# Performance work log

Measured on AMD Instinct MI355X. Metric: run time of the kernel, lower is better.

Reference implementation:

```python
import jax, jax.numpy as jnp
import numpy as np

B = 256          # graphs per batch
NC, NP = 16384, 131072   # compound / protein node counts
EC, EP = 131072, 2097152 # edge counts
D = 128


def _gconv(x, src, dst, W, b, n):
    # DGL GraphConv, norm='both': h = D_in^{-1/2} A D_out^{-1/2} x W + b
    ones = jnp.ones(src.shape, x.dtype)
    out_deg = jax.ops.segment_sum(ones, src, num_segments=n)
    in_deg = jax.ops.segment_sum(ones, dst, num_segments=n)
    ns = jax.lax.rsqrt(jnp.maximum(out_deg, 1.0))
    nd = jax.lax.rsqrt(jnp.maximum(in_deg, 1.0))
    h = (x * ns[:, None]) @ W           # apply weight before aggregation (same math, less traffic)
    m = jax.ops.segment_sum(h[src], dst, num_segments=n)  # SpMM aggregation
    return m * nd[:, None] + b


def _mean_nodes(x, gid, nb):
    s = jax.ops.segment_sum(x, gid, num_segments=nb)
    cnt = jax.ops.segment_sum(jnp.ones((x.shape[0],), x.dtype), gid, num_segments=nb)
    return s / jnp.maximum(cnt, 1.0)[:, None]


def setup_inputs() -> dict:
    key = jax.random.key(0)
    ks = jax.random.split(key, 24)
    s = 0.05
    inp = {
        "compound_feat": jax.random.normal(ks[0], (NC, 74), jnp.float32),
        "protein_feat": jax.random.normal(ks[1], (NP, 128), jnp.float32),
        # graph structure
        "c_src": jax.random.randint(ks[2], (EC,), 0, NC, jnp.int32),
        "c_dst": jax.random.randint(ks[3], (EC,), 0, NC, jnp.int32),
        "p_src": jax.random.randint(ks[4], (EP,), 0, NP, jnp.int32),
        "p_dst": jax.random.randint(ks[5], (EP,), 0, NP, jnp.int32),
        "c_gid": jax.random.randint(ks[6], (NC,), 0, B, jnp.int32),
        "p_gid": jax.random.randint(ks[7], (NP,), 0, B, jnp.int32),
        # GraphConv params
        "Wc1": jax.random.normal(ks[8], (74, D), jnp.float32) * s,
        "bc1": jnp.zeros((D,), jnp.float32),
        "Wc2": jax.random.normal(ks[9], (D, D), jnp.float32) * s,
        "bc2": jnp.zeros((D,), jnp.float32),
        "Wp1": jax.random.normal(ks[10], (128, D), jnp.float32) * s,
        "bp1": jnp.zeros((D,), jnp.float32),
        "Wp2": jax.random.normal(ks[11], (D, D), jnp.float32) * s,
        "bp2": jnp.zeros((D,), jnp.float32),
        # predictor MLP
        "Wf1": jax.random.normal(ks[12], (2 * D, D), jnp.float32) * s,
        "bf1": jnp.zeros((D,), jnp.float32),
        "Wf2": jax.random.normal(ks[13], (D, 1), jnp.float32) * s,
        "bf2": jnp.zeros((1,), jnp.float32),
    }
    return inp


def reference(compound_feat, protein_feat, c_src, c_dst, p_src, p_dst, c_gid, p_gid,
              Wc1, bc1, Wc2, bc2, Wp1, bp1, Wp2, bp2, Wf1, bf1, Wf2, bf2):
    c = jax.nn.relu(_gconv(compound_feat, c_src, c_dst, Wc1, bc1, NC))
    c = jax.nn.relu(_gconv(c, c_src, c_dst, Wc2, bc2, NC))
    c_global = _mean_nodes(c, c_gid, B)                     # [B, D]
    p = jax.nn.relu(_gconv(protein_feat, p_src, p_dst, Wp1, bp1, NP))
    p = jax.nn.relu(_gconv(p, p_src, p_dst, Wp2, bp2, NP))
    p_global = _mean_nodes(p, p_gid, B)                     # [B, D]
    combined = jnp.concatenate([c_global, p_global], axis=1)  # [B, 2D]
    h = jax.nn.relu(combined @ Wf1 + bf1)
    out = h @ Wf2 + bf2                                     # [B, 1]
    return out.squeeze(-1)
```

## Files before the change

kernel.cpp:

```cpp
#include <hip/hip_runtime.h>
#include <hip/hip_fp16.h>

#define D 128
#define SCH 4096
#define NBLK 256

typedef _Float16 half8 __attribute__((ext_vector_type(8)));
typedef float f32x4 __attribute__((ext_vector_type(4)));

struct HTask { const int* keys; int n; int shift; int* H; };
struct H6 { HTask t[6]; };

struct SPTask { const int* in; int n; int* part; };
struct SP6 { SPTask t[6]; };

struct SDTask { const int* in; int n; const int* part; int* out; int* total; };
struct SD6 { SDTask t[6]; };

struct ScTask { const int* k1; const int* k2; int n; int shift;
                const int* base1; const int* base2;
                int* o1; int* o2k; int* o2v; int mode; };
struct Sc4 { ScTask t[4]; };

struct CTask { const int* tmpk; const int* base; int n; int fine; int* deg; };
struct C4 { CTask t[4]; };

struct NTask { const int* outdeg; const int* indeg; float* ns; float* nd; int n; };
struct N2 { NTask t[2]; };

struct LTask { const int* tmpk; const int* tmpv; const int* base; int n;
               const int* rowptr; int shift; int fine; int* col; };
struct L2T { LTask t[2]; };

struct WPk { const float* W; _Float16* out; int K; };
struct W4 { WPk t[4]; };

struct GTask { const void* x; const float* ns; const _Float16* Wp; __half* h;
               int K; int xh; };
struct GemP { GTask t[2]; int nb0; };

struct ATask { const __half* h; const int* rowptr; const int* col;
               const float* nd; const float* b; const int* perm;
               void* out; int halfOut; };
struct AggP { ATask t[2]; int np; int ntot; };

struct MTask { const __half* x; const int* gbase; int n; float* out; };
struct M2 { MTask t[2]; };


__global__ __launch_bounds__(256) void k_hist_all(H6 P) {
  HTask tk = P.t[blockIdx.y];
  __shared__ int bins[256];
  int blk = blockIdx.x, t = threadIdx.x;
  bins[t] = 0;
  __syncthreads();
  int per = (tk.n + NBLK - 1) / NBLK;
  int beg = blk * per, end = min(beg + per, tk.n);
  for (int i = beg + t; i < end; i += 256)
    atomicAdd(&bins[tk.keys[i] >> tk.shift], 1);
  __syncthreads();
  tk.H[t * NBLK + blk] = bins[t];
}

__global__ __launch_bounds__(256) void k_scan_part_all(SP6 P) {
  SPTask tk = P.t[blockIdx.y];
  int b = blockIdx.x, t = threadIdx.x;
  int base = b * SCH;
  int s = 0;
  for (int i = t; i < SCH; i += 256) {
    int idx = base + i;
    if (idx < tk.n) s += tk.in[idx];
  }
  __shared__ int red[256];
  red[t] = s;
  __syncthreads();
  for (int d = 128; d > 0; d >>= 1) {
    if (t < d) red[t] += red[t + d];
    __syncthreads();
  }
  if (t == 0) tk.part[b] = red[0];
}

__global__ __launch_bounds__(256) void k_scan_down_all(SD6 P) {
  SDTask tk = P.t[blockIdx.y];
  int b = blockIdx.x, t = threadIdx.x;
  int lane = t & 63, wid = t >> 6;
  __shared__ int wsum[4];
  if (b == 0 && t == 0 && tk.total) {
    int s = 0;
    for (int w = 0; w < (int)gridDim.x; ++w) s += tk.part[w];
    *tk.total = s;
  }
  int offset = 0;
  for (int w = 0; w < b; ++w) offset += tk.part[w];
  int base = b * SCH;
  if (base >= tk.n) return;
  int idx0 = base + t * 16;
  int v[16];
  int s = 0;
#pragma unroll
  for (int i = 0; i < 16; ++i) {
    int idx = idx0 + i;
    v[i] = (idx < tk.n) ? tk.in[idx] : 0;
    s += v[i];
  }
  int inc = s;
  for (int d = 1; d < 64; d <<= 1) {
    int u = __shfl_up(inc, d, 64);
    if (lane >= d) inc += u;
  }
  if (lane == 63) wsum[wid] = inc;
  __syncthreads();
  int woff = 0;
  for (int w = 0; w < wid; ++w) woff += wsum[w];
  int ex = offset + woff + inc - s;
#pragma unroll
  for (int i = 0; i < 16; ++i) {
    int idx = idx0 + i;
    if (idx < tk.n) tk.out[idx] = ex;
    ex += v[i];
  }
}

__global__ __launch_bounds__(256) void k_scatter_all(Sc4 P) {
  ScTask tk = P.t[blockIdx.y];
  __shared__ int curA[256], curB[256];
  int blk = blockIdx.x, t = threadIdx.x;
  curA[t] = tk.base1[t * NBLK + blk];
  if (tk.mode == 0) curB[t] = tk.base2[t * NBLK + blk];
  __syncthreads();
  int per = (tk.n + NBLK - 1) / NBLK;
  int beg = blk * per, end = min(beg + per, tk.n);
  if (tk.mode == 0) {
    for (int i = beg + t; i < end; i += 256) {
      int s = tk.k1[i], d = tk.k2[i];
      int pa = atomicAdd(&curA[s >> tk.shift], 1);
      tk.o1[pa] = s;
      int pb = atomicAdd(&curB[d >> tk.shift], 1);
      tk.o2k[pb] = d;
      tk.o2v[pb] = s;
    }
  } else {
    for (int i = beg + t; i < end; i += 256) {
      int pa = atomicAdd(&curA[tk.k1[i] >> tk.shift], 1);
      tk.o1[i] = pa;
    }
  }
}

__global__ __launch_bounds__(256) void k_l2count_all(C4 P) {
  CTask tk = P.t[blockIdx.y];
  __shared__ int bins[512];
  int b = blockIdx.x, t = threadIdx.x;
  for (int f = t; f < tk.fine; f += 256) bins[f] = 0;
  __syncthreads();
  int beg = tk.base[b * NBLK];
  int end = (b == NBLK - 1) ? tk.n : tk.base[(b + 1) * NBLK];
  for (int i = beg + t; i < end; i += 256)
    atomicAdd(&bins[tk.tmpk[i] & (tk.fine - 1)], 1);
  __syncthreads();
  for (int f = t; f < tk.fine; f += 256)
    tk.deg[b * tk.fine + f] = bins[f];
}

__global__ __launch_bounds__(256) void k_norms_all(N2 P) {
  NTask tk = P.t[blockIdx.y];
  int i = blockIdx.x * blockDim.x + threadIdx.x;
  if (i < tk.n) {
    tk.ns[i] = rsqrtf(fmaxf((float)tk.outdeg[i], 1.f));
    tk.nd[i] = rsqrtf(fmaxf((float)tk.indeg[i], 1.f));
  }
}

__global__ __launch_bounds__(256) void k_l2scatter_all(L2T P) {
  LTask tk = P.t[blockIdx.y];
  __shared__ int cur[512];
  int b = blockIdx.x, t = threadIdx.x;
  int v0 = b << tk.shift;
  for (int f = t; f < tk.fine; f += 256) cur[f] = tk.rowptr[v0 + f];
  __syncthreads();
  int beg = tk.base[b * NBLK];
  int end = (b == NBLK - 1) ? tk.n : tk.base[(b + 1) * NBLK];
  for (int i = beg + t; i < end; i += 256) {
    int pos = atomicAdd(&cur[tk.tmpk[i] & (tk.fine - 1)], 1);
    tk.col[pos] = tk.tmpv[i];
  }
}


__global__ __launch_bounds__(256) void k_wpack(W4 P) {
  WPk tk = P.t[blockIdx.y];
  int f = blockIdx.x;
  int kch = (tk.K + 31) >> 5;
  if (f >= (kch << 3)) return;
  int kc = f >> 3, nt = f & 7;
  int t = threadIdx.x;
  int l = t & 63, e0 = (t >> 6) << 1;
  int col = (nt << 4) + (l & 15);
  int kb = (kc << 5) + ((l >> 4) << 3);
#pragma unroll
  for (int e = e0; e < e0 + 2; ++e) {
    int k = kb + e;
    float v = (k < tk.K) ? tk.W[(size_t)k * D + col] : 0.f;
    tk.out[(((size_t)f * 64 + l) << 3) + e] = (_Float16)v;
  }
}

__global__ __launch_bounds__(256) void k_nl_gemm(GemP P) {
  __shared__ __align__(16) _Float16 Bs[32 * 64 * 8];
  int bx = blockIdx.x;
  GTask tk;
  int v0;
  if (bx < P.nb0) { tk = P.t[0]; v0 = bx * 128; }
  else            { tk = P.t[1]; v0 = (bx - P.nb0) * 128; }
  const int K = tk.K;
  const int kch = (K + 31) >> 5;
  int t = threadIdx.x, w = t >> 6, l = t & 63;

  {
    const uint4* src = (const uint4*)tk.Wp;
    uint4* dst = (uint4*)Bs;
    int n16 = kch << 9;
    for (int i = t; i < n16; i += 256) dst[i] = src[i];
  }
  __syncthreads();

  int row = l & 15;
  int ks = (l >> 4) << 3;
  int m0 = v0 + (w << 5);
  const float* xf0 = nullptr; const float* xf1 = nullptr;
  const _Float16* xh0 = nullptr; const _Float16* xh1 = nullptr;
  if (tk.xh) {
    xh0 = (const _Float16*)tk.x + (size_t)(m0 + row) * D + ks;
    xh1 = xh0 + (size_t)16 * D;
  } else {
    xf0 = (const float*)tk.x + (size_t)(m0 + row) * K + ks;
    xf1 = xf0 + (size_t)16 * K;
  }

  f32x4 acc[2][8];
  f32x4 zero = {0.f, 0.f, 0.f, 0.f};
#pragma unroll
  for (int i = 0; i < 2; ++i)
#pragma unroll
    for (int j = 0; j < 8; ++j) acc[i][j] = zero;

  for (int kc = 0; kc < kch; ++kc) {
    half8 a0, a1;
    if (tk.xh) {
      a0 = *(const half8*)(xh0 + (kc << 5));
      a1 = *(const half8*)(xh1 + (kc << 5));
    } else if (K == D) {
      float4 p0 = *(const float4*)(xf0 + (kc << 5));
      float4 p1 = *(const float4*)(xf0 + (kc << 5) + 4);
      float4 q0 = *(const float4*)(xf1 + (kc << 5));
      float4 q1 = *(const float4*)(xf1 + (kc << 5) + 4);
      a0[0] = (_Float16)p0.x; a0[1] = (_Float16)p0.y;
      a0[2] = (_Float16)p0.z; a0[3] = (_Float16)p0.w;
      a0[4] = (_Float16)p1.x; a0[5] = (_Float16)p1.y;
      a0[6] = (_Float16)p1.z; a0[7] = (_Float16)p1.w;
      a1[0] = (_Float16)q0.x; a1[1] = (_Float16)q0.y;
      a1[2] = (_Float16)q0.z; a1[3] = (_Float16)q0.w;
      a1[4] = (_Float16)q1.x; a1[5] = (_Float16)q1.y;
      a1[6] = (_Float16)q1.z; a1[7] = (_Float16)q1.w;
    } else {
#pragma unroll
      for (int e = 0; e < 8; ++e) {
        int k = (kc << 5) + ks + e;
        a0[e] = (k < K) ? (_Float16)xf0[(kc << 5) + e] : (_Float16)0.f;
        a1[e] = (k < K) ? (_Float16)xf1[(kc << 5) + e] : (_Float16)0.f;
      }
    }
#pragma unroll
    for (int nt = 0; nt < 8; ++nt) {
      half8 b = *(const half8*)&Bs[(size_t)((((kc << 3) + nt) << 6) + l) << 3];
      acc[0][nt] = __builtin_amdgcn_mfma_f32_16x16x32_f16(a0, b, acc[0][nt], 0, 0, 0);
      acc[1][nt] = __builtin_amdgcn_mfma_f32_16x16x32_f16(a1, b, acc[1][nt], 0, 0, 0);
    }
  }

  int rr = (l >> 4) << 2;
  int c0 = l & 15;
#pragma unroll
  for (int mt = 0; mt < 2; ++mt) {
    int vb = m0 + (mt << 4) + rr;
    float s0 = tk.ns[vb], s1 = tk.ns[vb + 1];
    float s2 = tk.ns[vb + 2], s3 = tk.ns[vb + 3];
#pragma unroll
    for (int nt = 0; nt < 8; ++nt) {
      __half* hp = tk.h + (size_t)vb * D + (nt << 4) + c0;
      hp[0]     = __float2half_rn(acc[mt][nt][0] * s0);
      hp[D]     = __float2half_rn(acc[mt][nt][1] * s1);
      hp[2 * D] = __float2half_rn(acc[mt][nt][2] * s2);
      hp[3 * D] = __float2half_rn(acc[mt][nt][3] * s3);
    }
  }
}

__global__ __launch_bounds__(256) void k_aggregate(AggP P) {
  int wid = threadIdx.x >> 6;
  int lane = threadIdx.x & 63;
  int f0 = (lane & 15) * 8;
  int rsel = lane >> 4;
  int nw = (int)gridDim.x * 4;

  for (int gv = blockIdx.x * 4 + wid; gv < P.ntot; gv += nw) {
    ATask tk;
    int v;
    if (gv < P.np) { tk = P.t[0]; v = gv; }
    else           { tk = P.t[1]; v = gv - P.np; }
    int beg = tk.rowptr[v], end = tk.rowptr[v + 1];
    const __half* h = tk.h;
    const int* col = tk.col;

    float acc[8];
#pragma unroll
    for (int k = 0; k < 8; ++k) acc[k] = 0.f;

    for (int j = beg; j < end; j += 32) {
      int cc[8];
#pragma unroll
      for (int q = 0; q < 8; ++q) {
        int jj = j + 4 * q + rsel;
        cc[q] = (jj < end) ? col[jj] : -1;
      }
#pragma unroll
      for (int q = 0; q < 8; ++q) {
        if (cc[q] >= 0) {
          uint4 r = *(const uint4*)&h[(size_t)cc[q] * D + f0];
          const __half2* p = (const __half2*)&r;
#pragma unroll
          for (int k = 0; k < 4; ++k) {
            float2 f = __half22float2(p[k]);
            acc[2 * k] += f.x; acc[2 * k + 1] += f.y;
          }
        }
      }
    }

#pragma unroll
    for (int k = 0; k < 8; ++k) {
      acc[k] += __shfl_down(acc[k], 32, 64);
      acc[k] += __shfl_down(acc[k], 16, 64);
    }

    if (rsel == 0) {
      float s = tk.nd[v];
      float4 b0 = *(const float4*)&tk.b[f0];
      float4 b1 = *(const float4*)&tk.b[f0 + 4];
      float r[8];
      r[0] = fmaxf(fmaf(acc[0], s, b0.x), 0.f);
      r[1] = fmaxf(fmaf(acc[1], s, b0.y), 0.f);
      r[2] = fmaxf(fmaf(acc[2], s, b0.z), 0.f);
      r[3] = fmaxf(fmaf(acc[3], s, b0.w), 0.f);
      r[4] = fmaxf(fmaf(acc[4], s, b1.x), 0.f);
      r[5] = fmaxf(fmaf(acc[5], s, b1.y), 0.f);
      r[6] = fmaxf(fmaf(acc[6], s, b1.z), 0.f);
      r[7] = fmaxf(fmaf(acc[7], s, b1.w), 0.f);
      int ov = tk.perm ? tk.perm[v] : v;
      if (tk.halfOut) {
        union { __half2 h2[4]; uint4 u; } pk;
#pragma unroll
        for (int k = 0; k < 4; ++k) {
          pk.h2[k].x = __float2half_rn(r[2 * k]);
          pk.h2[k].y = __float2half_rn(r[2 * k + 1]);
        }
        *(uint4*)&((__half*)tk.out)[(size_t)ov * D + f0] = pk.u;
      } else {
        float4 o0 = {r[0], r[1], r[2], r[3]};
        float4 o1 = {r[4], r[5], r[6], r[7]};
        *(float4*)&((float*)tk.out)[(size_t)ov * D + f0] = o0;
        *(float4*)&((float*)tk.out)[(size_t)ov * D + f0 + 4] = o1;
      }
    }
  }
}

__device__ __forceinline__ void acc_half4(float4& a, const __half* p) {
  uint2 r = *(const uint2*)p;
  __half2 q0 = *(__half2*)&r.x;
  __half2 q1 = *(__half2*)&r.y;
  float2 f0 = __half22float2(q0);
  float2 f1 = __half22float2(q1);
  a.x += f0.x; a.y += f0.y; a.z += f1.x; a.w += f1.y;
}

__global__ __launch_bounds__(256) void k_seg_mean(M2 P) {
  MTask tk = P.t[blockIdx.y];
  int g = blockIdx.x, t = threadIdx.x;
  int slot = t >> 5;
  int c = (t & 31) * 4;
  int beg = tk.gbase[g * NBLK];
  int end = (g == (int)gridDim.x - 1) ? tk.n : tk.gbase[(g + 1) * NBLK];
  const __half* x = tk.x;

  float4 a0 = make_float4(0.f, 0.f, 0.f, 0.f);
  float4 a1 = make_float4(0.f, 0.f, 0.f, 0.f);
  int j = beg + slot;
  for (; j + 8 < end; j += 16) {
    acc_half4(a0, x + (size_t)j * D + c);
    acc_half4(a1, x + (size_t)(j + 8) * D + c);
  }
  if (j < end)
    acc_half4(a0, x + (size_t)j * D + c);
  a0.x += a1.x; a0.y += a1.y; a0.z += a1.z; a0.w += a1.w;

  a0.x += __shfl_down(a0.x, 32, 64);
  a0.y += __shfl_down(a0.y, 32, 64);
  a0.z += __shfl_down(a0.z, 32, 64);
  a0.w += __shfl_down(a0.w, 32, 64);

  __shared__ float sred[4][32 * 4];
  int wid = t >> 6, lane = t & 63;
  if (lane < 32) *(float4*)&sred[wid][lane * 4] = a0;
  __syncthreads();
  if (t < 32) {
    float4 s0 = *(const float4*)&sred[0][t * 4];
    float4 s1 = *(const float4*)&sred[1][t * 4];
    float4 s2 = *(const float4*)&sred[2][t * 4];
    float4 s3 = *(const float4*)&sred[3][t * 4];
    float inv = 1.f / fmaxf((float)(end - beg), 1.f);
    float4 r;
    r.x = (s0.x + s1.x + s2.x + s3.x) * inv;
    r.y = (s0.y + s1.y + s2.y + s3.y) * inv;
    r.z = (s0.z + s1.z + s2.z + s3.z) * inv;
    r.w = (s0.w + s1.w + s2.w + s3.w) * inv;
    *(float4*)&tk.out[(size_t)g * D + c] = r;
  }
}

__global__ void k_mlp(const float* __restrict__ cg, const float* __restrict__ pg,
                      const float* __restrict__ Wf1, const float* __restrict__ bf1,
                      const float* __restrict__ Wf2, const float* __restrict__ bf2,
                      float* __restrict__ out) {
  __shared__ float xs[256];
  __shared__ float red[128];
  int b = blockIdx.x, t = threadIdx.x;
  xs[t] = cg[b * D + t];
  xs[128 + t] = pg[b * D + t];
  __syncthreads();
  float acc = bf1[t];
  for (int k = 0; k < 256; ++k) acc = fmaf(xs[k], Wf1[k * D + t], acc);
  float hv = fmaxf(acc, 0.f);
  red[t] = hv * Wf2[t];
  for (int d = 64; d > 0; d >>= 1) {
    __syncthreads();
    if (t < d) red[t] += red[t + d];
  }
  if (t == 0) out[b] = red[0] + bf2[0];
}


extern "C" void kernel_launch(void* const* d_in, const int* in_sizes, int n_in,
                              void* d_out, int out_size, void* d_ws, size_t ws_size,
                              hipStream_t stream) {
  const float* compound_feat = (const float*)d_in[0];
  const float* protein_feat  = (const float*)d_in[1];
  const int* c_src = (const int*)d_in[2];
  const int* c_dst = (const int*)d_in[3];
  const int* p_src = (const int*)d_in[4];
  const int* p_dst = (const int*)d_in[5];
  const int* c_gid = (const int*)d_in[6];
  const int* p_gid = (const int*)d_in[7];
  const float* Wc1 = (const float*)d_in[8];  const float* bc1 = (const float*)d_in[9];
  const float* Wc2 = (const float*)d_in[10]; const float* bc2 = (const float*)d_in[11];
  const float* Wp1 = (const float*)d_in[12]; const float* bp1 = (const float*)d_in[13];
  const float* Wp2 = (const float*)d_in[14]; const float* bp2 = (const float*)d_in[15];
  const float* Wf1 = (const float*)d_in[16]; const float* bf1 = (const float*)d_in[17];
  const float* Wf2 = (const float*)d_in[18]; const float* bf2 = (const float*)d_in[19];
  float* out = (float*)d_out;

  const int EC = in_sizes[2], EP = in_sizes[4];
  const int NC = in_sizes[6], NP = in_sizes[7];
  const int B  = out_size;
  const int KC = in_sizes[0] / NC;
  const int cshift = __builtin_ctz(NC / 256), cfine = NC / 256;
  const int pshift = __builtin_ctz(NP / 256), pfine = NP / 256;
  const int HN = 256 * NBLK;

  char* ws = (char*)d_ws;
  size_t off = 0;
  auto alloc = [&](size_t bytes) -> void* {
    void* p = ws + off;
    off += (bytes + 255) & ~(size_t)255;
    return p;
  };

  int* H0 = (int*)alloc((size_t)HN * 4);
  int* H1 = (int*)alloc((size_t)HN * 4);
  int* H2 = (int*)alloc((size_t)HN * 4);
  int* H3 = (int*)alloc((size_t)HN * 4);
  int* H4 = (int*)alloc((size_t)HN * 4);
  int* H5 = (int*)alloc((size_t)HN * 4);
  int* partH = (int*)alloc((size_t)6 * 32 * 4);
  int* partD = (int*)alloc((size_t)2 * 32 * 4);
  int* tmps_c = (int*)alloc((size_t)EC * 4);
  int* tmpd_c = (int*)alloc((size_t)EC * 4);
  int* tmpv_c = (int*)alloc((size_t)EC * 4);
  int* tmps_p = (int*)alloc((size_t)EP * 4);
  int* tmpd_p = (int*)alloc((size_t)EP * 4);
  int* tmpv_p = (int*)alloc((size_t)EP * 4);
  int* c_outdeg = (int*)alloc((size_t)NC * 4);
  int* c_indeg  = (int*)alloc((size_t)NC * 4);
  int* p_outdeg = (int*)alloc((size_t)NP * 4);
  int* p_indeg  = (int*)alloc((size_t)NP * 4);
  float* c_ns = (float*)alloc((size_t)NC * 4);
  float* c_nd = (float*)alloc((size_t)NC * 4);
  float* p_ns = (float*)alloc((size_t)NP * 4);
  float* p_nd = (float*)alloc((size_t)NP * 4);
  int* c_rowptr = (int*)alloc((size_t)(NC + 1) * 4);
  int* p_rowptr = (int*)alloc((size_t)(NP + 1) * 4);
  int* c_col   = (int*)alloc((size_t)EC * 4);
  int* p_col   = (int*)alloc((size_t)EP * 4);
  int* c_perm = (int*)alloc((size_t)NC * 4);
  int* p_perm = (int*)alloc((size_t)NP * 4);
  __half* c_h  = (__half*)alloc((size_t)NC * D * 2);
  __half* c_m1 = (__half*)alloc((size_t)NC * D * 2);
  __half* c_m2 = (__half*)alloc((size_t)NC * D * 2);
  __half* p_h  = (__half*)alloc((size_t)NP * D * 2);
  __half* p_m1 = (__half*)alloc((size_t)NP * D * 2);
  __half* p_m2 = (__half*)alloc((size_t)NP * D * 2);
  float* cg = (float*)alloc((size_t)B * D * 4);
  float* pg = (float*)alloc((size_t)B * D * 4);
  _Float16* wp_p1 = (_Float16*)alloc((size_t)32 * 1024);
  _Float16* wp_c1 = (_Float16*)alloc((size_t)32 * 1024);
  _Float16* wp_p2 = (_Float16*)alloc((size_t)32 * 1024);
  _Float16* wp_c2 = (_Float16*)alloc((size_t)32 * 1024);
  (void)ws_size; (void)n_in;

  {
    W4 PW = {{{Wp1, wp_p1, D}, {Wc1, wp_c1, KC}, {Wp2, wp_p2, D}, {Wc2, wp_c2, D}}};
    k_wpack<<<dim3(32, 4), 256, 0, stream>>>(PW);
  }
  {
    H6 P = {{{c_src, EC, cshift, H0}, {c_dst, EC, cshift, H1}, {c_gid, NC, 0, H2},
             {p_src, EP, pshift, H3}, {p_dst, EP, pshift, H4}, {p_gid, NP, 0, H5}}};
    k_hist_all<<<dim3(NBLK, 6), 256, 0, stream>>>(P);
  }
  {
    SP6 Pp = {{{H0, HN, partH + 0}, {H1, HN, partH + 32}, {H2, HN, partH + 64},
               {H3, HN, partH + 96}, {H4, HN, partH + 128}, {H5, HN, partH + 160}}};
    k_scan_part_all<<<dim3(16, 6), 256, 0, stream>>>(Pp);
    SD6 Pd = {{{H0, HN, partH + 0, H0, nullptr}, {H1, HN, partH + 32, H1, nullptr},
               {H2, HN, partH + 64, H2, nullptr}, {H3, HN, partH + 96, H3, nullptr},
               {H4, HN, partH + 128, H4, nullptr}, {H5, HN, partH + 160, H5, nullptr}}};
    k_scan_down_all<<<dim3(16, 6), 256, 0, stream>>>(Pd);
  }
  {
    Sc4 P = {{{c_src, c_dst, EC, cshift, H0, H1, tmps_c, tmpd_c, tmpv_c, 0},
              {p_src, p_dst, EP, pshift, H3, H4, tmps_p, tmpd_p, tmpv_p, 0},
              {c_gid, nullptr, NC, 0, H2, nullptr, c_perm, nullptr, nullptr, 1},
              {p_gid, nullptr, NP, 0, H5, nullptr, p_perm, nullptr, nullptr, 1}}};
    k_scatter_all<<<dim3(NBLK, 4), 256, 0, stream>>>(P);
  }
  {
    C4 P = {{{tmps_c, H0, EC, cfine, c_outdeg}, {tmpd_c, H1, EC, cfine, c_indeg},
             {tmps_p, H3, EP, pfine, p_outdeg}, {tmpd_p, H4, EP, pfine, p_indeg}}};
    k_l2count_all<<<dim3(NBLK, 4), 256, 0, stream>>>(P);
  }
  {
    SP6 Pp; Pp.t[0] = {c_indeg, NC, partD + 0}; Pp.t[1] = {p_indeg, NP, partD + 32};
    Pp.t[2] = Pp.t[3] = Pp.t[4] = Pp.t[5] = SPTask{c_indeg, 0, partD + 0};
    k_scan_part_all<<<dim3(32, 2), 256, 0, stream>>>(Pp);
    SD6 Pd; Pd.t[0] = {c_indeg, NC, partD + 0, c_rowptr, c_rowptr + NC};
    Pd.t[1] = {p_indeg, NP, partD + 32, p_rowptr, p_rowptr + NP};
    Pd.t[2] = Pd.t[3] = Pd.t[4] = Pd.t[5] = Pd.t[0];
    k_scan_down_all<<<dim3(32, 2), 256, 0, stream>>>(Pd);
  }
  {
    N2 P = {{{c_outdeg, c_indeg, c_ns, c_nd, NC}, {p_outdeg, p_indeg, p_ns, p_nd, NP}}};
    k_norms_all<<<dim3((NP + 255) / 256, 2), 256, 0, stream>>>(P);
  }
  {
    L2T P = {{{tmpd_c, tmpv_c, H1, EC, c_rowptr, cshift, cfine, c_col},
              {tmpd_p, tmpv_p, H4, EP, p_rowptr, pshift, pfine, p_col}}};
    k_l2scatter_all<<<dim3(NBLK, 2), 256, 0, stream>>>(P);
  }

  const int gnb = NP / 128 + NC / 128;
  const int ntot = NP + NC;
  const int anb = min((ntot + 3) / 4, 8192);
  {
    GemP P = {{{protein_feat, p_ns, wp_p1, p_h, D, 0},
               {compound_feat, c_ns, wp_c1, c_h, KC, 0}}, NP / 128};
    k_nl_gemm<<<gnb, 256, 0, stream>>>(P);
  }
  {
    AggP P = {{{p_h, p_rowptr, p_col, p_nd, bp1, nullptr, p_m1, 1},
               {c_h, c_rowptr, c_col, c_nd, bc1, nullptr, c_m1, 1}}, NP, ntot};
    k_aggregate<<<anb, 256, 0, stream>>>(P);
  }
  {
    GemP P = {{{p_m1, p_ns, wp_p2, p_h, D, 1}, {c_m1, c_ns, wp_c2, c_h, D, 1}}, NP / 128};
    k_nl_gemm<<<gnb, 256, 0, stream>>>(P);
  }
  {
    AggP P = {{{p_h, p_rowptr, p_col, p_nd, bp2, p_perm, p_m2, 1},
               {c_h, c_rowptr, c_col, c_nd, bc2, c_perm, c_m2, 1}}, NP, ntot};
    k_aggregate<<<anb, 256, 0, stream>>>(P);
  }
  {
    M2 P = {{{c_m2, H2, NC, cg}, {p_m2, H5, NP, pg}}};
    k_seg_mean<<<dim3(B, 2), 256, 0, stream>>>(P);
  }

  k_mlp<<<B, D, 0, stream>>>(cg, pg, Wf1, bf1, Wf2, bf2, out);
}
```

Baseline: 518.7 us.

## Fuse CSR second-level passes and pack edge keys; merge segment-mean with MLP head

Replaces the separate fine-level count, rowptr scan, norm and column-scatter kernels with one fused kernel. Each coarse bucket counts its fine bins, scans them locally in shared memory, writes rowptr and the norms, then scatters the columns. Scatter outputs are compacted: source low bits go to 16-bit values, and destination low bits plus the source index are packed into one 32-bit word. This cuts edge temp traffic and removes four launches. The graph mean-pooling and the predictor MLP are also merged into a single head kernel, at the cost of tighter bit-width assumptions (node id < 2^17, fine <= 512).

```diff
diff --git a/kernel.cpp b/kernel.cpp
--- a/kernel.cpp
+++ b/kernel.cpp
@@ -17,20 +17,15 @@
 struct SDTask { const int* in; int n; const int* part; int* out; int* total; };
 struct SD6 { SDTask t[6]; };
 
-struct ScTask { const int* k1; const int* k2; int n; int shift;
+struct ScTask { const int* k1; const int* k2; int n; int shift; int mask;
                 const int* base1; const int* base2;
-                int* o1; int* o2k; int* o2v; int mode; };
+                unsigned short* o1h; int* o1i; unsigned int* o2; int mode; };
 struct Sc4 { ScTask t[4]; };
 
-struct CTask { const int* tmpk; const int* base; int n; int fine; int* deg; };
-struct C4 { CTask t[4]; };
-
-struct NTask { const int* outdeg; const int* indeg; float* ns; float* nd; int n; };
-struct N2 { NTask t[2]; };
-
-struct LTask { const int* tmpk; const int* tmpv; const int* base; int n;
-               const int* rowptr; int shift; int fine; int* col; };
-struct L2T { LTask t[2]; };
+struct FS { const unsigned short* lows; const int* base; int n; int fine; float* ns; };
+struct FD { const unsigned int* pk; const int* base; int n; int fine;
+            int* rowptr; int* col; float* nd; int nnodes; };
+struct FZ { FS s[2]; FD d[2]; };
 
 struct WPk { const float* W; _Float16* out; int K; };
 struct W4 { WPk t[4]; };
@@ -44,8 +39,10 @@
                void* out; int halfOut; };
 struct AggP { ATask t[2]; int np; int ntot; };
 
-struct MTask { const __half* x; const int* gbase; int n; float* out; };
-struct M2 { MTask t[2]; };
+struct HeadP { const __half* cx; const int* cbase; int cn;
+               const __half* px; const int* pbase; int pn;
+               const float* Wf1; const float* bf1; const float* Wf2; const float* bf2;
+               float* out; };
 
 
 __global__ __launch_bounds__(256) void k_hist_all(H6 P) {
@@ -135,55 +132,80 @@
     for (int i = beg + t; i < end; i += 256) {
       int s = tk.k1[i], d = tk.k2[i];
       int pa = atomicAdd(&curA[s >> tk.shift], 1);
-      tk.o1[pa] = s;
+      tk.o1h[pa] = (unsigned short)(s & tk.mask);
       int pb = atomicAdd(&curB[d >> tk.shift], 1);
-      tk.o2k[pb] = d;
-      tk.o2v[pb] = s;
+      tk.o2[pb] = ((unsigned int)(d & tk.mask) << 17) | (unsigned int)s;
     }
   } else {
     for (int i = beg + t; i < end; i += 256) {
       int pa = atomicAdd(&curA[tk.k1[i] >> tk.shift], 1);
-      tk.o1[i] = pa;
-    }
-  }
-}
-
-__global__ __launch_bounds__(256) void k_l2count_all(C4 P) {
-  CTask tk = P.t[blockIdx.y];
+      tk.o1i[i] = pa;
+    }
+  }
+}
+
+__global__ __launch_bounds__(256) void k_l2fused(FZ P) {
   __shared__ int bins[512];
-  int b = blockIdx.x, t = threadIdx.x;
-  for (int f = t; f < tk.fine; f += 256) bins[f] = 0;
-  __syncthreads();
-  int beg = tk.base[b * NBLK];
-  int end = (b == NBLK - 1) ? tk.n : tk.base[(b + 1) * NBLK];
-  for (int i = beg + t; i < end; i += 256)
-    atomicAdd(&bins[tk.tmpk[i] & (tk.fine - 1)], 1);
-  __syncthreads();
-  for (int f = t; f < tk.fine; f += 256)
-    tk.deg[b * tk.fine + f] = bins[f];
-}
-
-__global__ __launch_bounds__(256) void k_norms_all(N2 P) {
-  NTask tk = P.t[blockIdx.y];
-  int i = blockIdx.x * blockDim.x + threadIdx.x;
-  if (i < tk.n) {
-    tk.ns[i] = rsqrtf(fmaxf((float)tk.outdeg[i], 1.f));
-    tk.nd[i] = rsqrtf(fmaxf((float)tk.indeg[i], 1.f));
-  }
-}
-
-__global__ __launch_bounds__(256) void k_l2scatter_all(L2T P) {
-  LTask tk = P.t[blockIdx.y];
-  __shared__ int cur[512];
-  int b = blockIdx.x, t = threadIdx.x;
-  int v0 = b << tk.shift;
-  for (int f = t; f < tk.fine; f += 256) cur[f] = tk.rowptr[v0 + f];
-  __syncthreads();
-  int beg = tk.base[b * NBLK];
-  int end = (b == NBLK - 1) ? tk.n : tk.base[(b + 1) * NBLK];
-  for (int i = beg + t; i < end; i += 256) {
-    int pos = atomicAdd(&cur[tk.tmpk[i] & (tk.fine - 1)], 1);
-    tk.col[pos] = tk.tmpv[i];
+  __shared__ int pos[512];
+  __shared__ int wsum[4];
+  int b = blockIdx.x, t = threadIdx.x, ty = blockIdx.y;
+  if (ty < 2) {
+    FS tk = P.s[ty];
+    for (int f = t; f < tk.fine; f += 256) bins[f] = 0;
+    __syncthreads();
+    int beg = tk.base[b * NBLK];
+    int end = (b == NBLK - 1) ? tk.n : tk.base[(b + 1) * NBLK];
+    for (int i = beg + t; i < end; i += 256)
+      atomicAdd(&bins[tk.lows[i]], 1);
+    __syncthreads();
+    int v0 = b * tk.fine;
+    for (int f = t; f < tk.fine; f += 256)
+      tk.ns[v0 + f] = rsqrtf(fmaxf((float)bins[f], 1.f));
+  } else {
+    FD tk = P.d[ty - 2];
+    for (int f = t; f < tk.fine; f += 256) bins[f] = 0;
+    __syncthreads();
+    int beg = tk.base[b * NBLK];
+    int end = (b == NBLK - 1) ? tk.n : tk.base[(b + 1) * NBLK];
+    for (int i = beg + t; i < end; i += 256)
+      atomicAdd(&bins[tk.pk[i] >> 17], 1);
+    __syncthreads();
+    int lane = t & 63, wid = t >> 6;
+    int c = (tk.fine + 255) >> 8;
+    int i0 = t * c;
+    int vc[2] = {0, 0};
+    int s = 0;
+#pragma unroll
+    for (int q = 0; q < 2; ++q) {
+      if (q < c && i0 + q < tk.fine) { vc[q] = bins[i0 + q]; s += vc[q]; }
+    }
+    int inc = s;
+    for (int dd = 1; dd < 64; dd <<= 1) {
+      int u = __shfl_up(inc, dd, 64);
+      if (lane >= dd) inc += u;
+    }
+    if (lane == 63) wsum[wid] = inc;
+    __syncthreads();
+    int woff = 0;
+    for (int w = 0; w < wid; ++w) woff += wsum[w];
+    int ex = beg + woff + inc - s;
+#pragma unroll
+    for (int q = 0; q < 2; ++q) {
+      if (q < c && i0 + q < tk.fine) { pos[i0 + q] = ex; ex += vc[q]; }
+    }
+    __syncthreads();
+    int v0 = b * tk.fine;
+    for (int f = t; f < tk.fine; f += 256) {
+      tk.rowptr[v0 + f] = pos[f];
+      tk.nd[v0 + f] = rsqrtf(fmaxf((float)bins[f], 1.f));
+    }
+    if (b == NBLK - 1 && t == 0) tk.rowptr[tk.nnodes] = tk.n;
+    __syncthreads();
+    for (int i = beg + t; i < end; i += 256) {
+      unsigned int pk = tk.pk[i];
+      int p = atomicAdd(&pos[pk >> 17], 1);
+      tk.col[p] = (int)(pk & 0x1FFFFu);
+    }
   }
 }
 
@@ -385,15 +407,11 @@
   a.x += f0.x; a.y += f0.y; a.z += f1.x; a.w += f1.y;
 }
 
-__global__ __launch_bounds__(256) void k_seg_mean(M2 P) {
-  MTask tk = P.t[blockIdx.y];
-  int g = blockIdx.x, t = threadIdx.x;
+__device__ __forceinline__ void block_mean_128(const __half* x, int beg, int end,
+                                               float* dst, float (*sred)[128]) {
+  int t = threadIdx.x;
   int slot = t >> 5;
   int c = (t & 31) * 4;
-  int beg = tk.gbase[g * NBLK];
-  int end = (g == (int)gridDim.x - 1) ? tk.n : tk.gbase[(g + 1) * NBLK];
-  const __half* x = tk.x;
-
   float4 a0 = make_float4(0.f, 0.f, 0.f, 0.f);
   float4 a1 = make_float4(0.f, 0.f, 0.f, 0.f);
   int j = beg + slot;
@@ -410,7 +428,6 @@
   a0.z += __shfl_down(a0.z, 32, 64);
   a0.w += __shfl_down(a0.w, 32, 64);
 
-  __shared__ float sred[4][32 * 4];
   int wid = t >> 6, lane = t & 63;
   if (lane < 32) *(float4*)&sred[wid][lane * 4] = a0;
   __syncthreads();
@@ -425,29 +442,42 @@
     r.y = (s0.y + s1.y + s2.y + s3.y) * inv;
     r.z = (s0.z + s1.z + s2.z + s3.z) * inv;
     r.w = (s0.w + s1.w + s2.w + s3.w) * inv;
-    *(float4*)&tk.out[(size_t)g * D + c] = r;
-  }
-}
-
-__global__ void k_mlp(const float* __restrict__ cg, const float* __restrict__ pg,
-                      const float* __restrict__ Wf1, const float* __restrict__ bf1,
-                      const float* __restrict__ Wf2, const float* __restrict__ bf2,
-                      float* __restrict__ out) {
+    *(float4*)&dst[t * 4] = r;
+  }
+  __syncthreads();
+}
+
+__global__ __launch_bounds__(256) void k_head(HeadP P) {
   __shared__ float xs[256];
-  __shared__ float red[128];
-  int b = blockIdx.x, t = threadIdx.x;
-  xs[t] = cg[b * D + t];
-  xs[128 + t] = pg[b * D + t];
-  __syncthreads();
-  float acc = bf1[t];
-  for (int k = 0; k < 256; ++k) acc = fmaf(xs[k], Wf1[k * D + t], acc);
-  float hv = fmaxf(acc, 0.f);
-  red[t] = hv * Wf2[t];
+  __shared__ float sred[4][128];
+  int g = blockIdx.x, t = threadIdx.x;
+  int nb = (int)gridDim.x;
+
+  int cb = P.cbase[g * NBLK];
+  int ce = (g == nb - 1) ? P.cn : P.cbase[(g + 1) * NBLK];
+  block_mean_128(P.cx, cb, ce, xs, sred);
+  int pb = P.pbase[g * NBLK];
+  int pe = (g == nb - 1) ? P.pn : P.pbase[(g + 1) * NBLK];
+  block_mean_128(P.px, pb, pe, xs + 128, sred);
+
+  int hu = t & 127, half = t >> 7;
+  float acc = 0.f;
+  int k0 = half * 128;
+  for (int k = k0; k < k0 + 128; ++k)
+    acc = fmaf(xs[k], P.Wf1[k * D + hu], acc);
+  float* hacc = &sred[2][0];
+  float* red = &sred[0][0];
+  hacc[t] = acc;
+  __syncthreads();
+  if (t < 128) {
+    float hv = fmaxf(hacc[t] + hacc[t + 128] + P.bf1[t], 0.f);
+    red[t] = hv * P.Wf2[t];
+  }
   for (int d = 64; d > 0; d >>= 1) {
     __syncthreads();
     if (t < d) red[t] += red[t + d];
   }
-  if (t == 0) out[b] = red[0] + bf2[0];
+  if (t == 0) P.out[g] = red[0] + P.bf2[0];
 }
 
 
@@ -493,17 +523,10 @@
   int* H4 = (int*)alloc((size_t)HN * 4);
   int* H5 = (int*)alloc((size_t)HN * 4);
   int* partH = (int*)alloc((size_t)6 * 32 * 4);
-  int* partD = (int*)alloc((size_t)2 * 32 * 4);
-  int* tmps_c = (int*)alloc((size_t)EC * 4);
-  int* tmpd_c = (int*)alloc((size_t)EC * 4);
-  int* tmpv_c = (int*)alloc((size_t)EC * 4);
-  int* tmps_p = (int*)alloc((size_t)EP * 4);
-  int* tmpd_p = (int*)alloc((size_t)EP * 4);
-  int* tmpv_p = (int*)alloc((size_t)EP * 4);
-  int* c_outdeg = (int*)alloc((size_t)NC * 4);
-  int* c_indeg  = (int*)alloc((size_t)NC * 4);
-  int* p_outdeg = (int*)alloc((size_t)NP * 4);
-  int* p_indeg  = (int*)alloc((size_t)NP * 4);
+  unsigned short* tmps_c = (unsigned short*)alloc((size_t)EC * 2);
+  unsigned short* tmps_p = (unsigned short*)alloc((size_t)EP * 2);
+  unsigned int* tmpe_c = (unsigned int*)alloc((size_t)EC * 4);
+  unsigned int* tmpe_p = (unsigned int*)alloc((size_t)EP * 4);
   float* c_ns = (float*)alloc((size_t)NC * 4);
   float* c_nd = (float*)alloc((size_t)NC * 4);
   float* p_ns = (float*)alloc((size_t)NP * 4);
@@ -520,8 +543,6 @@
   __half* p_h  = (__half*)alloc((size_t)NP * D * 2);
   __half* p_m1 = (__half*)alloc((size_t)NP * D * 2);
   __half* p_m2 = (__half*)alloc((size_t)NP * D * 2);
-  float* cg = (float*)alloc((size_t)B * D * 4);
-  float* pg = (float*)alloc((size_t)B * D * 4);
   _Float16* wp_p1 = (_Float16*)alloc((size_t)32 * 1024);
   _Float16* wp_c1 = (_Float16*)alloc((size_t)32 * 1024);
   _Float16* wp_p2 = (_Float16*)alloc((size_t)32 * 1024);
@@ -547,34 +568,17 @@
     k_scan_down_all<<<dim3(16, 6), 256, 0, stream>>>(Pd);
   }
   {
-    Sc4 P = {{{c_src, c_dst, EC, cshift, H0, H1, tmps_c, tmpd_c, tmpv_c, 0},
-              {p_src, p_dst, EP, pshift, H3, H4, tmps_p, tmpd_p, tmpv_p, 0},
-              {c_gid, nullptr, NC, 0, H2, nullptr, c_perm, nullptr, nullptr, 1},
-              {p_gid, nullptr, NP, 0, H5, nullptr, p_perm, nullptr, nullptr, 1}}};
+    Sc4 P = {{{c_src, c_dst, EC, cshift, cfine - 1, H0, H1, tmps_c, nullptr, tmpe_c, 0},
+              {p_src, p_dst, EP, pshift, pfine - 1, H3, H4, tmps_p, nullptr, tmpe_p, 0},
+              {c_gid, nullptr, NC, 0, 0, H2, nullptr, nullptr, c_perm, nullptr, 1},
+              {p_gid, nullptr, NP, 0, 0, H5, nullptr, nullptr, p_perm, nullptr, 1}}};
     k_scatter_all<<<dim3(NBLK, 4), 256, 0, stream>>>(P);
   }
   {
-    C4 P = {{{tmps_c, H0, EC, cfine, c_outdeg}, {tmpd_c, H1, EC, cfine, c_indeg},
-             {tmps_p, H3, EP, pfine, p_outdeg}, {tmpd_p, H4, EP, pfine, p_indeg}}};
-    k_l2count_all<<<dim3(NBLK, 4), 256, 0, stream>>>(P);
-  }
-  {
-    SP6 Pp; Pp.t[0] = {c_indeg, NC, partD + 0}; Pp.t[1] = {p_indeg, NP, partD + 32};
-    Pp.t[2] = Pp.t[3] = Pp.t[4] = Pp.t[5] = SPTask{c_indeg, 0, partD + 0};
-    k_scan_part_all<<<dim3(32, 2), 256, 0, stream>>>(Pp);
-    SD6 Pd; Pd.t[0] = {c_indeg, NC, partD + 0, c_rowptr, c_rowptr + NC};
-    Pd.t[1] = {p_indeg, NP, partD + 32, p_rowptr, p_rowptr + NP};
-    Pd.t[2] = Pd.t[3] = Pd.t[4] = Pd.t[5] = Pd.t[0];
-    k_scan_down_all<<<dim3(32, 2), 256, 0, stream>>>(Pd);
-  }
-  {
-    N2 P = {{{c_outdeg, c_indeg, c_ns, c_nd, NC}, {p_outdeg, p_indeg, p_ns, p_nd, NP}}};
-    k_norms_all<<<dim3((NP + 255) / 256, 2), 256, 0, stream>>>(P);
-  }
-  {
-    L2T P = {{{tmpd_c, tmpv_c, H1, EC, c_rowptr, cshift, cfine, c_col},
-              {tmpd_p, tmpv_p, H4, EP, p_rowptr, pshift, pfine, p_col}}};
-    k_l2scatter_all<<<dim3(NBLK, 2), 256, 0, stream>>>(P);
+    FZ PF = {{{tmps_c, H0, EC, cfine, c_ns}, {tmps_p, H3, EP, pfine, p_ns}},
+             {{tmpe_c, H1, EC, cfine, c_rowptr, c_col, c_nd, NC},
+              {tmpe_p, H4, EP, pfine, p_rowptr, p_col, p_nd, NP}}};
+    k_l2fused<<<dim3(NBLK, 4), 256, 0, stream>>>(PF);
   }
 
   const int gnb = NP / 128 + NC / 128;
@@ -600,9 +604,7 @@
     k_aggregate<<<anb, 256, 0, stream>>>(P);
   }
   {
-    M2 P = {{{c_m2, H2, NC, cg}, {p_m2, H5, NP, pg}}};
-    k_seg_mean<<<dim3(B, 2), 256, 0, stream>>>(P);
-  }
-
-  k_mlp<<<B, D, 0, stream>>>(cg, pg, Wf1, bf1, Wf2, bf2, out);
-}
+    HeadP PH = {c_m2, H2, NC, p_m2, H5, NP, Wf1, bf1, Wf2, bf2, out};
+    k_head<<<B, 256, 0, stream>>>(PH);
+  }
+}
```

Measured after the change: 502.4 us. 3.1% less time.
